# Optimization experiments

Hardware: AMD Instinct MI355X
Metric: run time of the kernel (lower is better)

The kernel has to match this reference:

```python
import jax, jax.numpy as jnp
import numpy as np
import itertools

DIM = 192          # channels
H = W = 64         # input_resolution
WS = 7             # window_size
NH = 6             # num_heads
KD = DIM // NH     # key_dim = 32
D = KD             # attn_ratio=1 -> d = key_dim
DH = D * NH        # 192
B = 16             # batch
HID = int(DIM * 4.0)  # mlp hidden = 768
EPS = 1e-5


def _build_bias_idxs():
    points = list(itertools.product(range(WS), range(WS)))
    offsets, idxs = {}, []
    for p1 in points:
        for p2 in points:
            off = (abs(p1[0] - p2[0]), abs(p1[1] - p2[1]))
            if off not in offsets:
                offsets[off] = len(offsets)
            idxs.append(offsets[off])
    return np.array(idxs, dtype=np.int32).reshape(len(points), len(points)), len(offsets)


def _ln(x, w, b):
    m = x.mean(-1, keepdims=True)
    v = ((x - m) ** 2).mean(-1, keepdims=True)
    return (x - m) * jax.lax.rsqrt(v + EPS) * w + b


def setup_inputs():
    key = jax.random.key(0)
    ks = jax.random.split(key, 20)
    n = lambda k, s, sc=0.02: jax.random.normal(k, s, jnp.float32) * sc
    idxs_np, n_off = _build_bias_idxs()  # [49,49], 49 offsets
    qkv_out = DH + 2 * KD * NH  # 576
    return {
        "x": jax.random.normal(ks[0], (B, H * W, DIM), jnp.float32),
        "ln1_w": jnp.ones((DIM,), jnp.float32),
        "ln1_b": jnp.zeros((DIM,), jnp.float32),
        "qkv_w": n(ks[1], (DIM, qkv_out)),
        "qkv_b": jnp.zeros((qkv_out,), jnp.float32),
        "attn_biases": n(ks[2], (NH, n_off), 0.1),
        "proj_w": n(ks[3], (DH, DIM)),
        "proj_b": jnp.zeros((DIM,), jnp.float32),
        "conv_w": n(ks[4], (DIM, 1, 3, 3), 0.1),  # depthwise OIHW
        "bn_g": jnp.ones((DIM,), jnp.float32),
        "bn_b": jnp.zeros((DIM,), jnp.float32),
        "bn_m": n(ks[5], (DIM,), 0.01),
        "bn_v": jax.random.uniform(ks[6], (DIM,), jnp.float32, 0.5, 1.5),
        "ln2_w": jnp.ones((DIM,), jnp.float32),
        "ln2_b": jnp.zeros((DIM,), jnp.float32),
        "fc1_w": n(ks[7], (DIM, HID)),
        "fc1_b": jnp.zeros((HID,), jnp.float32),
        "fc2_w": n(ks[8], (HID, DIM)),
        "fc2_b": jnp.zeros((DIM,), jnp.float32),
        "bias_idxs": jnp.asarray(idxs_np),
    }


def reference(x, ln1_w, ln1_b, qkv_w, qkv_b, attn_biases, proj_w, proj_b,
              conv_w, bn_g, bn_b, bn_m, bn_v, ln2_w, ln2_b,
              fc1_w, fc1_b, fc2_w, fc2_b, bias_idxs):
    Bn, N, C = x.shape
    shortcut = x

    # ---- window partition (pad 64 -> 70, 10x10 windows of 7x7) ----
    pad = (WS - H % WS) % WS  # 6
    pH = H + pad
    nW = pH // WS  # 10
    xw = x.reshape(Bn, H, W, C)
    xw = jnp.pad(xw, ((0, 0), (0, pad), (0, pad), (0, 0)))
    xw = xw.reshape(Bn, nW, WS, nW, WS, C).transpose(0, 1, 3, 2, 4, 5)
    xw = xw.reshape(Bn * nW * nW, WS * WS, C)  # [1600, 49, C]

    # ---- attention with relative position bias ----
    xn = _ln(xw, ln1_w, ln1_b)
    qkv = xn @ qkv_w + qkv_b                     # [Bw, 49, 576]
    qkv = qkv.reshape(-1, WS * WS, NH, KD + KD + D)
    q, k, v = jnp.split(qkv, [KD, 2 * KD], axis=3)
    q = q.transpose(0, 2, 1, 3)  # [Bw, NH, 49, KD]
    k = k.transpose(0, 2, 1, 3)
    v = v.transpose(0, 2, 1, 3)
    bias = attn_biases[:, bias_idxs]             # [NH, 49, 49]
    attn = jnp.einsum('bhqd,bhkd->bhqk', q, k) * (KD ** -0.5) + bias
    attn = jax.nn.softmax(attn, axis=-1)
    out = jnp.einsum('bhqk,bhkd->bhqd', attn, v)
    out = out.transpose(0, 2, 1, 3).reshape(-1, WS * WS, DH)
    out = out @ proj_w + proj_b                  # [Bw, 49, C]

    # ---- window reverse + unpad ----
    out = out.reshape(Bn, nW, nW, WS, WS, C).transpose(0, 1, 3, 2, 4, 5)
    out = out.reshape(Bn, pH, pH, C)[:, :H, :W].reshape(Bn, N, C)

    x = shortcut + out

    # ---- depthwise local conv + BN (eval) ----
    xc = x.transpose(0, 2, 1).reshape(Bn, C, H, W)
    y = jax.lax.conv_general_dilated(
        xc, conv_w, (1, 1), [(1, 1), (1, 1)],
        dimension_numbers=('NCHW', 'OIHW', 'NCHW'), feature_group_count=C)
    scale = bn_g * jax.lax.rsqrt(bn_v + EPS)
    y = y * scale[None, :, None, None] + (bn_b - bn_m * scale)[None, :, None, None]
    x = y.reshape(Bn, C, N).transpose(0, 2, 1)

    # ---- MLP with pre-LN residual ----
    h = _ln(x, ln2_w, ln2_b)
    h = jax.nn.gelu(h @ fc1_w + fc1_b, approximate=False)
    h = h @ fc2_w + fc2_b
    return x + h
```

## Files before the change

kernel.cpp:

```cpp
#include <hip/hip_runtime.h>
#include <hip/hip_bf16.h>

#define C 192
#define NHh 6
#define NT 49
#define IMG 64
#define WSZ 7

#define XS2 200
#define QKS 392
#define VTS 72
#define PLS 72
#define X3S 200

typedef __attribute__((ext_vector_type(8))) short bf16x8;
typedef __attribute__((ext_vector_type(4))) float f32x4;

__device__ __forceinline__ float bf2f(unsigned short u) {
    union { unsigned int i; float f; } v; v.i = ((unsigned int)u) << 16; return v.f;
}
__device__ __forceinline__ unsigned short f2bf(float f) {
    __hip_bfloat16 h = __float2bfloat16(f);
    return *(unsigned short*)&h;
}
__device__ __forceinline__ float gelu_f(float v) {
    return 0.5f * v * (1.f + erff(v * 0.70710678118654752f));
}

__global__ __launch_bounds__(256) void prep_kernel(
    const float* __restrict__ fc1_w, const float* __restrict__ fc2_w,
    const float* __restrict__ qkv_w, const float* __restrict__ proj_w,
    const float* __restrict__ biases, int noff, const int* __restrict__ bidx,
    const float* __restrict__ bn_g, const float* __restrict__ bn_b,
    const float* __restrict__ bn_m, const float* __restrict__ bn_v,
    unsigned short* __restrict__ wfc1t, unsigned short* __restrict__ wfc2t,
    unsigned short* __restrict__ wqkvt, unsigned short* __restrict__ wprojt,
    float* __restrict__ biasfp, float* __restrict__ bnsc, float* __restrict__ bnsh)
{
    int i = blockIdx.x * 256 + threadIdx.x;
    if (i < 147456) {
        int k = i / 768, n = i - k * 768;
        wfc1t[n * 192 + k] = f2bf(fc1_w[i]);
    } else if (i < 294912) {
        int j = i - 147456;
        int k = j / 192, n = j - k * 192;
        wfc2t[n * 768 + k] = f2bf(fc2_w[j]);
    } else if (i < 405504) {
        int j = i - 294912;
        int k = j / 576, n = j - k * 576;
        wqkvt[n * 192 + k] = f2bf(qkv_w[j]);
    } else if (i < 442368) {
        int j = i - 405504;
        int k = j / 192, n = j - k * 192;
        wprojt[n * 192 + k] = f2bf(proj_w[j]);
    } else if (i < 466944) {
        int j = i - 442368;
        int h = j >> 12, rem = j & 4095;
        int q = rem >> 6, k = rem & 63;
        biasfp[j] = (q < NT && k < NT) ? biases[h * noff + bidx[q * NT + k]] : -1.0e30f;
    } else if (i < 467136) {
        int c = i - 466944;
        float sc = bn_g[c] * rsqrtf(bn_v[c] + 1e-5f);
        bnsc[c] = sc;
        bnsh[c] = bn_b[c] - bn_m[c] * sc;
    }
}

__global__ __launch_bounds__(512) void attn_win_mfma(
    const float* __restrict__ x,
    const float* __restrict__ ln1_w, const float* __restrict__ ln1_b,
    const unsigned short* __restrict__ wqkvt, const float* __restrict__ qkv_b,
    const float* __restrict__ biasfp,
    const unsigned short* __restrict__ wprojt, const float* __restrict__ proj_b,
    unsigned short* __restrict__ x2)
{
    extern __shared__ char smem[];
    unsigned short* xn = (unsigned short*)smem;
    unsigned short* qk = (unsigned short*)(smem + 25600);
    unsigned short* vt = (unsigned short*)(smem + 75776);
    unsigned short* pl = (unsigned short*)(smem + 103424);
    float* stats = (float*)(smem + 121856);

    const int tid = threadIdx.x;
    const int blk = blockIdx.x;
    const int b  = blk / 100;
    const int wi = (blk / 10) % 10;
    const int wj = blk % 10;
    const size_t base = (size_t)b * 4096;
    const int wid = tid >> 6, lane = tid & 63, lr = lane & 15, lg = lane >> 4;

    for (int idx = tid; idx < 64*48; idx += 512) {
        int t = idx / 48, c0 = (idx - t*48) * 4;
        ushort4 sv; sv.x = 0; sv.y = 0; sv.z = 0; sv.w = 0;
        if (t < NT) {
            int gh = wi*WSZ + t/WSZ, gw = wj*WSZ + t%WSZ;
            if (gh < IMG && gw < IMG) {
                float4 v = *(const float4*)(x + (base + (size_t)(gh*IMG + gw))*C + c0);
                sv.x = f2bf(v.x); sv.y = f2bf(v.y); sv.z = f2bf(v.z); sv.w = f2bf(v.w);
            }
        }
        *(ushort4*)&xn[t*XS2 + c0] = sv;
    }
    __syncthreads();

    {
        int lt = tid >> 3, sl = tid & 7;
        float s = 0.f, s2 = 0.f;
        for (int c = sl; c < C; c += 8) {
            float v = bf2f(xn[lt*XS2 + c]);
            s += v; s2 += v*v;
        }
        #pragma unroll
        for (int msk = 1; msk < 8; msk <<= 1) {
            s  += __shfl_xor(s,  msk, 64);
            s2 += __shfl_xor(s2, msk, 64);
        }
        if (sl == 0) {
            float m = s * (1.f/C), var = s2 * (1.f/C) - m*m;
            stats[2*lt]   = m;
            stats[2*lt+1] = rsqrtf(var + 1e-5f);
        }
    }
    __syncthreads();

    for (int idx = tid; idx < 64*48; idx += 512) {
        int t = idx / 48, c0 = (idx - t*48) * 4;
        float mm = stats[2*t], rr = stats[2*t+1];
        ushort4 sv = *(ushort4*)&xn[t*XS2 + c0];
        sv.x = f2bf((bf2f(sv.x) - mm) * rr * ln1_w[c0+0] + ln1_b[c0+0]);
        sv.y = f2bf((bf2f(sv.y) - mm) * rr * ln1_w[c0+1] + ln1_b[c0+1]);
        sv.z = f2bf((bf2f(sv.z) - mm) * rr * ln1_w[c0+2] + ln1_b[c0+2]);
        sv.w = f2bf((bf2f(sv.w) - mm) * rr * ln1_w[c0+3] + ln1_b[c0+3]);
        *(ushort4*)&xn[t*XS2 + c0] = sv;
    }
    __syncthreads();

    for (int nt = wid; nt < 36; nt += 8) {
        const int ncol = nt*16 + lr;
        f32x4 acc0 = {0.f,0.f,0.f,0.f}, acc1 = {0.f,0.f,0.f,0.f};
        f32x4 acc2 = {0.f,0.f,0.f,0.f}, acc3 = {0.f,0.f,0.f,0.f};
        const unsigned short* wp = wqkvt + ncol*192 + lg*8;
        #pragma unroll
        for (int ks = 0; ks < 6; ++ks) {
            bf16x8 bfr = *(const bf16x8*)(wp + ks*32);
            bf16x8 a0 = *(const bf16x8*)(xn + (0*16+lr)*XS2 + ks*32 + lg*8);
            bf16x8 a1 = *(const bf16x8*)(xn + (1*16+lr)*XS2 + ks*32 + lg*8);
            bf16x8 a2 = *(const bf16x8*)(xn + (2*16+lr)*XS2 + ks*32 + lg*8);
            bf16x8 a3 = *(const bf16x8*)(xn + (3*16+lr)*XS2 + ks*32 + lg*8);
            acc0 = __builtin_amdgcn_mfma_f32_16x16x32_bf16(a0, bfr, acc0, 0, 0, 0);
            acc1 = __builtin_amdgcn_mfma_f32_16x16x32_bf16(a1, bfr, acc1, 0, 0, 0);
            acc2 = __builtin_amdgcn_mfma_f32_16x16x32_bf16(a2, bfr, acc2, 0, 0, 0);
            acc3 = __builtin_amdgcn_mfma_f32_16x16x32_bf16(a3, bfr, acc3, 0, 0, 0);
        }
        float bias = qkv_b[ncol];
        const int h = ncol / 96, wo = ncol - h*96;
        #pragma unroll
        for (int mt = 0; mt < 4; ++mt) {
            f32x4 av = (mt==0) ? acc0 : (mt==1) ? acc1 : (mt==2) ? acc2 : acc3;
            #pragma unroll
            for (int r = 0; r < 4; ++r) {
                int tok = mt*16 + lg*4 + r;
                unsigned short v = f2bf(av[r] + bias);
                if (wo < 64) qk[tok*QKS + h*64 + wo] = v;
                else         vt[(h*32 + (wo-64))*VTS + tok] = v;
            }
        }
    }
    __syncthreads();

    unsigned short* ao = xn;
    for (int u = wid; u < 24; u += 8) {
        const int h = u >> 2, nq = u & 3;
        const int qg = nq*16 + lr;
        f32x4 s0 = {0.f,0.f,0.f,0.f}, s1 = {0.f,0.f,0.f,0.f};
        f32x4 s2 = {0.f,0.f,0.f,0.f}, s3 = {0.f,0.f,0.f,0.f};
        bf16x8 qf = *(const bf16x8*)(qk + qg*QKS + h*64 + lg*8);
        bf16x8 k0 = *(const bf16x8*)(qk + (0*16+lr)*QKS + h*64 + 32 + lg*8);
        bf16x8 k1 = *(const bf16x8*)(qk + (1*16+lr)*QKS + h*64 + 32 + lg*8);
        bf16x8 k2 = *(const bf16x8*)(qk + (2*16+lr)*QKS + h*64 + 32 + lg*8);
        bf16x8 k3 = *(const bf16x8*)(qk + (3*16+lr)*QKS + h*64 + 32 + lg*8);
        s0 = __builtin_amdgcn_mfma_f32_16x16x32_bf16(k0, qf, s0, 0, 0, 0);
        s1 = __builtin_amdgcn_mfma_f32_16x16x32_bf16(k1, qf, s1, 0, 0, 0);
        s2 = __builtin_amdgcn_mfma_f32_16x16x32_bf16(k2, qf, s2, 0, 0, 0);
        s3 = __builtin_amdgcn_mfma_f32_16x16x32_bf16(k3, qf, s3, 0, 0, 0);
        const float* bp = biasfp + (size_t)(h*64 + qg)*64 + lg*4;
        float sv[4][4];
        float mx = -3.0e38f;
        #pragma unroll
        for (int mk = 0; mk < 4; ++mk) {
            f32x4 sa = (mk==0) ? s0 : (mk==1) ? s1 : (mk==2) ? s2 : s3;
            float4 b4 = *(const float4*)(bp + mk*16);
            sv[mk][0] = sa[0] * 0.17677669529663687f + b4.x;
            sv[mk][1] = sa[1] * 0.17677669529663687f + b4.y;
            sv[mk][2] = sa[2] * 0.17677669529663687f + b4.z;
            sv[mk][3] = sa[3] * 0.17677669529663687f + b4.w;
            #pragma unroll
            for (int r = 0; r < 4; ++r) mx = fmaxf(mx, sv[mk][r]);
        }
        mx = fmaxf(mx, __shfl_xor(mx, 16, 64));
        mx = fmaxf(mx, __shfl_xor(mx, 32, 64));
        float sum = 0.f;
        #pragma unroll
        for (int mk = 0; mk < 4; ++mk)
            #pragma unroll
            for (int r = 0; r < 4; ++r) { sv[mk][r] = __expf(sv[mk][r] - mx); sum += sv[mk][r]; }
        sum += __shfl_xor(sum, 16, 64);
        sum += __shfl_xor(sum, 32, 64);
        float inv = 1.f / sum;
        unsigned short* pw = pl + (wid*16 + lr)*PLS;
        #pragma unroll
        for (int mk = 0; mk < 4; ++mk)
            #pragma unroll
            for (int r = 0; r < 4; ++r) pw[mk*16 + lg*4 + r] = f2bf(sv[mk][r] * inv);
        #pragma unroll
        for (int dt = 0; dt < 2; ++dt) {
            f32x4 oa = {0.f,0.f,0.f,0.f};
            #pragma unroll
            for (int kk = 0; kk < 2; ++kk) {
                bf16x8 vf = *(const bf16x8*)(vt + (h*32 + dt*16 + lr)*VTS + kk*32 + lg*8);
                bf16x8 pf = *(const bf16x8*)(pl + (wid*16 + lr)*PLS + kk*32 + lg*8);
                oa = __builtin_amdgcn_mfma_f32_16x16x32_bf16(vf, pf, oa, 0, 0, 0);
            }
            #pragma unroll
            for (int r = 0; r < 4; ++r)
                ao[(nq*16 + lr)*XS2 + h*32 + dt*16 + lg*4 + r] = f2bf(oa[r]);
        }
    }
    __syncthreads();

    for (int nt = wid; nt < 12; nt += 8) {
        const int ncol = nt*16 + lr;
        f32x4 acc0 = {0.f,0.f,0.f,0.f}, acc1 = {0.f,0.f,0.f,0.f};
        f32x4 acc2 = {0.f,0.f,0.f,0.f}, acc3 = {0.f,0.f,0.f,0.f};
        const unsigned short* wp = wprojt + ncol*192 + lg*8;
        #pragma unroll
        for (int ks = 0; ks < 6; ++ks) {
            bf16x8 bfr = *(const bf16x8*)(wp + ks*32);
            bf16x8 a0 = *(const bf16x8*)(ao + (0*16+lr)*XS2 + ks*32 + lg*8);
            bf16x8 a1 = *(const bf16x8*)(ao + (1*16+lr)*XS2 + ks*32 + lg*8);
            bf16x8 a2 = *(const bf16x8*)(ao + (2*16+lr)*XS2 + ks*32 + lg*8);
            bf16x8 a3 = *(const bf16x8*)(ao + (3*16+lr)*XS2 + ks*32 + lg*8);
            acc0 = __builtin_amdgcn_mfma_f32_16x16x32_bf16(a0, bfr, acc0, 0, 0, 0);
            acc1 = __builtin_amdgcn_mfma_f32_16x16x32_bf16(a1, bfr, acc1, 0, 0, 0);
            acc2 = __builtin_amdgcn_mfma_f32_16x16x32_bf16(a2, bfr, acc2, 0, 0, 0);
            acc3 = __builtin_amdgcn_mfma_f32_16x16x32_bf16(a3, bfr, acc3, 0, 0, 0);
        }
        float bias = proj_b[ncol];
        #pragma unroll
        for (int mt = 0; mt < 4; ++mt) {
            f32x4 av = (mt==0) ? acc0 : (mt==1) ? acc1 : (mt==2) ? acc2 : acc3;
            #pragma unroll
            for (int r = 0; r < 4; ++r) {
                int tok = mt*16 + lg*4 + r;
                if (tok >= NT) continue;
                int gh = wi*WSZ + tok/WSZ, gw = wj*WSZ + tok%WSZ;
                if (gh >= IMG || gw >= IMG) continue;
                size_t g = (base + (size_t)(gh*IMG + gw))*C + ncol;
                x2[g] = f2bf(av[r] + bias + x[g]);
            }
        }
    }
}

__device__ __forceinline__ f32x4 mfma16(bf16x8 a, bf16x8 b, f32x4 c) {
    return __builtin_amdgcn_mfma_f32_16x16x32_bf16(a, b, c, 0, 0, 0);
}

__device__ __forceinline__ void mlp_produce(
    int ch, unsigned short* buf, const unsigned short* xnl,
    const unsigned short* __restrict__ wfc1t, const float* __restrict__ fc1_b,
    int wid, int lr, int lk)
{
    bf16x8 xa0[6], xa1[6];
    #pragma unroll
    for (int ks = 0; ks < 6; ++ks) {
        xa0[ks] = *(const bf16x8*)(xnl + lr*X3S + ks*32 + lk*8);
        xa1[ks] = *(const bf16x8*)(xnl + (16+lr)*X3S + ks*32 + lk*8);
    }
    #pragma unroll
    for (int t = 0; t < 3; ++t) {
        const int nl = (wid*3 + t)*16 + lr;
        const int ncol = ch*192 + nl;
        f32x4 a0 = {0.f,0.f,0.f,0.f}, a1 = {0.f,0.f,0.f,0.f};
        const unsigned short* wp = wfc1t + (size_t)ncol*192 + lk*8;
        #pragma unroll
        for (int ks = 0; ks < 6; ++ks) {
            bf16x8 bfr = *(const bf16x8*)(wp + ks*32);
            a0 = mfma16(xa0[ks], bfr, a0);
            a1 = mfma16(xa1[ks], bfr, a1);
        }
        float bias = fc1_b[ncol];
        #pragma unroll
        for (int r = 0; r < 4; ++r) {
            int row0 = lk*4 + r;
            buf[row0*X3S + nl]      = f2bf(gelu_f(a0[r] + bias));
            buf[(row0+16)*X3S + nl] = f2bf(gelu_f(a1[r] + bias));
        }
    }
}

__device__ __forceinline__ void mlp_consume(
    int ch, const unsigned short* buf,
    const unsigned short* __restrict__ wfc2t,
    f32x4* acc0, f32x4* acc1, int nb2, int lr, int lk)
{
    #pragma unroll
    for (int ks = 0; ks < 6; ++ks) {
        bf16x8 af0 = *(const bf16x8*)(buf + lr*X3S + ks*32 + lk*8);
        bf16x8 af1 = *(const bf16x8*)(buf + (16+lr)*X3S + ks*32 + lk*8);
        #pragma unroll
        for (int n = 0; n < 3; ++n) {
            bf16x8 b = *(const bf16x8*)(wfc2t + (size_t)(nb2 + n*16 + lr)*768 + ch*192 + ks*32 + lk*8);
            acc0[n] = mfma16(af0, b, acc0[n]);
            acc1[n] = mfma16(af1, b, acc1[n]);
        }
    }
}

__global__ __launch_bounds__(256) void conv_mlp2(
    const unsigned short* __restrict__ x2,
    const float* __restrict__ conv_w,
    const float* __restrict__ bnsc, const float* __restrict__ bnsh,
    const float* __restrict__ ln2_w, const float* __restrict__ ln2_b,
    const unsigned short* __restrict__ wfc1t, const float* __restrict__ fc1_b,
    const unsigned short* __restrict__ wfc2t, const float* __restrict__ fc2_b,
    float* __restrict__ out)
{
    extern __shared__ char smem[];
    unsigned short* x3  = (unsigned short*)smem;
    unsigned short* xnl = (unsigned short*)(smem + 12800);
    unsigned short* h1a = (unsigned short*)(smem + 25600);
    unsigned short* h1b = (unsigned short*)(smem + 38400);
    float* stats = (float*)(smem + 51200);

    const int tid  = threadIdx.x;
    const int base = blockIdx.x * 32;
    const int b    = base >> 12;
    const int n0   = base & 4095;
    const int hh   = n0 >> 6;
    const int w0v  = n0 & 63;
    const size_t ibase = (size_t)b * 4096;

    for (int idx = tid; idx < 32*48; idx += 256) {
        int lt = idx / 48, c0 = (idx - lt*48) * 4;
        int ww = w0v + lt;
        float a0 = 0.f, a1 = 0.f, a2 = 0.f, a3 = 0.f;
        #pragma unroll
        for (int kh = -1; kh <= 1; ++kh) {
            int h2 = hh + kh;
            if (h2 < 0 || h2 >= IMG) continue;
            #pragma unroll
            for (int kw = -1; kw <= 1; ++kw) {
                int w2 = ww + kw;
                if (w2 < 0 || w2 >= IMG) continue;
                ushort4 v = *(const ushort4*)(x2 + (ibase + (size_t)(h2*IMG + w2))*C + c0);
                int tap = (kh+1)*3 + (kw+1);
                a0 += bf2f(v.x) * conv_w[(c0+0)*9 + tap];
                a1 += bf2f(v.y) * conv_w[(c0+1)*9 + tap];
                a2 += bf2f(v.z) * conv_w[(c0+2)*9 + tap];
                a3 += bf2f(v.w) * conv_w[(c0+3)*9 + tap];
            }
        }
        ushort4 o;
        o.x = f2bf(a0 * bnsc[c0+0] + bnsh[c0+0]);
        o.y = f2bf(a1 * bnsc[c0+1] + bnsh[c0+1]);
        o.z = f2bf(a2 * bnsc[c0+2] + bnsh[c0+2]);
        o.w = f2bf(a3 * bnsc[c0+3] + bnsh[c0+3]);
        *(ushort4*)&x3[lt*X3S + c0] = o;
    }
    __syncthreads();

    {
        int lt = tid >> 3, sl = tid & 7;
        float s = 0.f, s2 = 0.f;
        for (int c = sl; c < C; c += 8) {
            float v = bf2f(x3[lt*X3S + c]);
            s += v; s2 += v*v;
        }
        #pragma unroll
        for (int msk = 1; msk < 8; msk <<= 1) {
            s  += __shfl_xor(s,  msk, 64);
            s2 += __shfl_xor(s2, msk, 64);
        }
        if (sl == 0) {
            float m = s * (1.f/C), var = s2 * (1.f/C) - m*m;
            stats[2*lt]   = m;
            stats[2*lt+1] = rsqrtf(var + 1e-5f);
        }
    }
    __syncthreads();

    for (int idx = tid; idx < 32*48; idx += 256) {
        int lt = idx / 48, c0 = (idx - lt*48) * 4;
        float mm = stats[2*lt], rr = stats[2*lt+1];
        ushort4 v = *(ushort4*)&x3[lt*X3S + c0];
        ushort4 sv;
        sv.x = f2bf((bf2f(v.x) - mm) * rr * ln2_w[c0+0] + ln2_b[c0+0]);
        sv.y = f2bf((bf2f(v.y) - mm) * rr * ln2_w[c0+1] + ln2_b[c0+1]);
        sv.z = f2bf((bf2f(v.z) - mm) * rr * ln2_w[c0+2] + ln2_b[c0+2]);
        sv.w = f2bf((bf2f(v.w) - mm) * rr * ln2_w[c0+3] + ln2_b[c0+3]);
        *(ushort4*)&xnl[lt*XS2 + c0] = sv;
    }
    __syncthreads();

    const int wid = tid >> 6, l = tid & 63, lr = l & 15, lk = l >> 4;
    const int nb2 = wid * 48;

    f32x4 acc0[3] = {{0.f,0.f,0.f,0.f},{0.f,0.f,0.f,0.f},{0.f,0.f,0.f,0.f}};
    f32x4 acc1[3] = {{0.f,0.f,0.f,0.f},{0.f,0.f,0.f,0.f},{0.f,0.f,0.f,0.f}};

    mlp_produce(0, h1a, xnl, wfc1t, fc1_b, wid, lr, lk);
    __syncthreads();

    mlp_produce(1, h1b, xnl, wfc1t, fc1_b, wid, lr, lk);
    mlp_consume(0, h1a, wfc2t, acc0, acc1, nb2, lr, lk);
    __syncthreads();

    mlp_produce(2, h1a, xnl, wfc1t, fc1_b, wid, lr, lk);
    mlp_consume(1, h1b, wfc2t, acc0, acc1, nb2, lr, lk);
    __syncthreads();

    mlp_produce(3, h1b, xnl, wfc1t, fc1_b, wid, lr, lk);
    mlp_consume(2, h1a, wfc2t, acc0, acc1, nb2, lr, lk);
    __syncthreads();

    mlp_consume(3, h1b, wfc2t, acc0, acc1, nb2, lr, lk);

    #pragma unroll
    for (int n = 0; n < 3; ++n) {
        int col = nb2 + n*16 + lr;
        float bias = fc2_b[col];
        #pragma unroll
        for (int r = 0; r < 4; ++r) {
            int row0 = lk*4 + r;
            float v0 = acc0[n][r] + bias + bf2f(x3[row0*X3S + col]);
            float v1 = acc1[n][r] + bias + bf2f(x3[(row0+16)*X3S + col]);
            out[(size_t)(base + row0) * C + col]      = v0;
            out[(size_t)(base + row0 + 16) * C + col] = v1;
        }
    }
}

extern "C" void kernel_launch(void* const* d_in, const int* in_sizes, int n_in,
                              void* d_out, int out_size, void* d_ws, size_t ws_size,
                              hipStream_t stream)
{
    const float* x      = (const float*)d_in[0];
    const float* ln1_w  = (const float*)d_in[1];
    const float* ln1_b  = (const float*)d_in[2];
    const float* qkv_w  = (const float*)d_in[3];
    const float* qkv_b  = (const float*)d_in[4];
    const float* biases = (const float*)d_in[5];
    const float* proj_w = (const float*)d_in[6];
    const float* proj_b = (const float*)d_in[7];
    const float* conv_w = (const float*)d_in[8];
    const float* bn_g   = (const float*)d_in[9];
    const float* bn_b   = (const float*)d_in[10];
    const float* bn_m   = (const float*)d_in[11];
    const float* bn_v   = (const float*)d_in[12];
    const float* ln2_w  = (const float*)d_in[13];
    const float* ln2_b  = (const float*)d_in[14];
    const float* fc1_w  = (const float*)d_in[15];
    const float* fc1_b  = (const float*)d_in[16];
    const float* fc2_w  = (const float*)d_in[17];
    const float* fc2_b  = (const float*)d_in[18];
    const int* bidx     = (const int*)d_in[19];

    char* ws = (char*)d_ws;
    unsigned short* x2    = (unsigned short*)ws;
    unsigned short* wfc1t = (unsigned short*)(ws + 25165824);
    unsigned short* wfc2t = (unsigned short*)(ws + 25460736);
    unsigned short* wqkvt = (unsigned short*)(ws + 25755648);
    unsigned short* wprojt= (unsigned short*)(ws + 25976832);
    float*          biasfp= (float*)(ws + 26050560);
    float*          bnsc  = (float*)(ws + 26148864);
    float*          bnsh  = (float*)(ws + 26149632);
    float* out = (float*)d_out;
    int noff = in_sizes[5] / NHh;

    prep_kernel<<<(467136 + 255)/256, 256, 0, stream>>>(
        fc1_w, fc2_w, qkv_w, proj_w, biases, noff, bidx,
        bn_g, bn_b, bn_m, bn_v,
        wfc1t, wfc2t, wqkvt, wprojt, biasfp, bnsc, bnsh);

    size_t smem1 = 122368;
    hipFuncSetAttribute((const void*)attn_win_mfma,
                        hipFuncAttributeMaxDynamicSharedMemorySize, (int)smem1);
    attn_win_mfma<<<16*100, 512, smem1, stream>>>(
        x, ln1_w, ln1_b, wqkvt, qkv_b, biasfp, wprojt, proj_b, x2);

    size_t smem2 = 51456;
    hipFuncSetAttribute((const void*)conv_mlp2,
                        hipFuncAttributeMaxDynamicSharedMemorySize, (int)smem2);
    conv_mlp2<<<65536/32, 256, smem2, stream>>>(
        x2, conv_w, bnsc, bnsh, ln2_w, ln2_b,
        wfc1t, fc1_b, wfc2t, fc2_b, out);
}
```

Measured before the change: 552.2 us.

## Tile-transpose weight prep, keep conv output in registers, stash residual in output

```diff
diff --git a/kernel.cpp b/kernel.cpp
--- a/kernel.cpp
+++ b/kernel.cpp
@@ -33,36 +33,56 @@
     const float* __restrict__ biases, int noff, const int* __restrict__ bidx,
     const float* __restrict__ bn_g, const float* __restrict__ bn_b,
     const float* __restrict__ bn_m, const float* __restrict__ bn_v,
+    const float* __restrict__ conv_w,
     unsigned short* __restrict__ wfc1t, unsigned short* __restrict__ wfc2t,
     unsigned short* __restrict__ wqkvt, unsigned short* __restrict__ wprojt,
-    float* __restrict__ biasfp, float* __restrict__ bnsc, float* __restrict__ bnsh)
+    float* __restrict__ biasfp, float* __restrict__ bnsc, float* __restrict__ bnsh,
+    float* __restrict__ convwt)
 {
-    int i = blockIdx.x * 256 + threadIdx.x;
-    if (i < 147456) {
-        int k = i / 768, n = i - k * 768;
-        wfc1t[n * 192 + k] = f2bf(fc1_w[i]);
-    } else if (i < 294912) {
-        int j = i - 147456;
-        int k = j / 192, n = j - k * 192;
-        wfc2t[n * 768 + k] = f2bf(fc2_w[j]);
-    } else if (i < 405504) {
-        int j = i - 294912;
-        int k = j / 576, n = j - k * 576;
-        wqkvt[n * 192 + k] = f2bf(qkv_w[j]);
-    } else if (i < 442368) {
-        int j = i - 405504;
-        int k = j / 192, n = j - k * 192;
-        wprojt[n * 192 + k] = f2bf(proj_w[j]);
-    } else if (i < 466944) {
-        int j = i - 442368;
-        int h = j >> 12, rem = j & 4095;
-        int q = rem >> 6, k = rem & 63;
-        biasfp[j] = (q < NT && k < NT) ? biases[h * noff + bidx[q * NT + k]] : -1.0e30f;
-    } else if (i < 467136) {
-        int c = i - 466944;
-        float sc = bn_g[c] * rsqrtf(bn_v[c] + 1e-5f);
-        bnsc[c] = sc;
-        bnsh[c] = bn_b[c] - bn_m[c] * sc;
+    __shared__ unsigned short tbuf[64 * 68];
+    const int bid = blockIdx.x, tid = threadIdx.x;
+
+    if (bid < 108) {
+        const float* src; unsigned short* dst; int K, N, tk, tn;
+        if (bid < 36)      { src = fc1_w;  dst = wfc1t;  K = 192; N = 768; tk = bid/12;      tn = bid%12; }
+        else if (bid < 72) { src = fc2_w;  dst = wfc2t;  K = 768; N = 192; tk = (bid-36)/3;  tn = (bid-36)%3; }
+        else if (bid < 99) { src = qkv_w;  dst = wqkvt;  K = 192; N = 576; tk = (bid-72)/9;  tn = (bid-72)%9; }
+        else               { src = proj_w; dst = wprojt; K = 192; N = 192; tk = (bid-99)/3;  tn = (bid-99)%3; }
+        for (int i = tid; i < 1024; i += 256) {
+            int r = i >> 4, c = (i & 15) * 4;
+            float4 v = *(const float4*)(src + (size_t)(tk*64 + r) * N + tn*64 + c);
+            ushort4 s; s.x = f2bf(v.x); s.y = f2bf(v.y); s.z = f2bf(v.z); s.w = f2bf(v.w);
+            *(ushort4*)&tbuf[r*68 + c] = s;
+        }
+        __syncthreads();
+        for (int i = tid; i < 1024; i += 256) {
+            int n = i >> 4, k = (i & 15) * 4;
+            ushort4 o;
+            o.x = tbuf[(k+0)*68 + n];
+            o.y = tbuf[(k+1)*68 + n];
+            o.z = tbuf[(k+2)*68 + n];
+            o.w = tbuf[(k+3)*68 + n];
+            *(ushort4*)(dst + (size_t)(tn*64 + n) * K + tk*64 + k) = o;
+        }
+    } else if (bid < 204) {
+        int j = (bid - 108) * 256 + tid;
+        if (j < 24576) {
+            int h = j >> 12, rem = j & 4095;
+            int q = rem >> 6, k = rem & 63;
+            biasfp[j] = (q < NT && k < NT) ? biases[h * noff + bidx[q * NT + k]] : -1.0e30f;
+        }
+    } else {
+        for (int it = tid; it < 1920; it += 256) {
+            if (it < 192) {
+                float sc = bn_g[it] * rsqrtf(bn_v[it] + 1e-5f);
+                bnsc[it] = sc;
+                bnsh[it] = bn_b[it] - bn_m[it] * sc;
+            } else {
+                int idx = it - 192;
+                int tap = idx / 192, c = idx - tap * 192;
+                convwt[tap * 192 + c] = conv_w[c * 9 + tap];
+            }
+        }
     }
 }
 
@@ -317,21 +337,19 @@
     }
 }
 
-__global__ __launch_bounds__(256) void conv_mlp2(
+__global__ __launch_bounds__(256, 4) void conv_mlp3(
     const unsigned short* __restrict__ x2,
-    const float* __restrict__ conv_w,
+    const float* __restrict__ convwt,
     const float* __restrict__ bnsc, const float* __restrict__ bnsh,
     const float* __restrict__ ln2_w, const float* __restrict__ ln2_b,
     const unsigned short* __restrict__ wfc1t, const float* __restrict__ fc1_b,
     const unsigned short* __restrict__ wfc2t, const float* __restrict__ fc2_b,
-    float* __restrict__ out)
+    float* out)
 {
     extern __shared__ char smem[];
-    unsigned short* x3  = (unsigned short*)smem;
-    unsigned short* xnl = (unsigned short*)(smem + 12800);
-    unsigned short* h1a = (unsigned short*)(smem + 25600);
-    unsigned short* h1b = (unsigned short*)(smem + 38400);
-    float* stats = (float*)(smem + 51200);
+    unsigned short* xnl = (unsigned short*)smem;
+    unsigned short* h1a = (unsigned short*)(smem + 12800);
+    unsigned short* h1b = (unsigned short*)(smem + 25600);
 
     const int tid  = threadIdx.x;
     const int base = blockIdx.x * 32;
@@ -341,10 +359,12 @@
     const int w0v  = n0 & 63;
     const size_t ibase = (size_t)b * 4096;
 
-    for (int idx = tid; idx < 32*48; idx += 256) {
-        int lt = idx / 48, c0 = (idx - lt*48) * 4;
-        int ww = w0v + lt;
-        float a0 = 0.f, a1 = 0.f, a2 = 0.f, a3 = 0.f;
+    {
+        const int lt = tid >> 3, sl = tid & 7;
+        const int ww = w0v + lt;
+        float4 xv[6];
+        #pragma unroll
+        for (int j = 0; j < 6; ++j) { xv[j].x = 0.f; xv[j].y = 0.f; xv[j].z = 0.f; xv[j].w = 0.f; }
         #pragma unroll
         for (int kh = -1; kh <= 1; ++kh) {
             int h2 = hh + kh;
@@ -353,53 +373,53 @@
             for (int kw = -1; kw <= 1; ++kw) {
                 int w2 = ww + kw;
                 if (w2 < 0 || w2 >= IMG) continue;
-                ushort4 v = *(const ushort4*)(x2 + (ibase + (size_t)(h2*IMG + w2))*C + c0);
-                int tap = (kh+1)*3 + (kw+1);
-                a0 += bf2f(v.x) * conv_w[(c0+0)*9 + tap];
-                a1 += bf2f(v.y) * conv_w[(c0+1)*9 + tap];
-                a2 += bf2f(v.z) * conv_w[(c0+2)*9 + tap];
-                a3 += bf2f(v.w) * conv_w[(c0+3)*9 + tap];
+                const unsigned short* src = x2 + (ibase + (size_t)(h2*IMG + w2))*C;
+                const float* wt = convwt + ((kh+1)*3 + (kw+1)) * 192;
+                #pragma unroll
+                for (int j = 0; j < 6; ++j) {
+                    int c0 = (sl + 8*j) * 4;
+                    ushort4 v = *(const ushort4*)(src + c0);
+                    float4 w = *(const float4*)(wt + c0);
+                    xv[j].x += bf2f(v.x) * w.x;
+                    xv[j].y += bf2f(v.y) * w.y;
+                    xv[j].z += bf2f(v.z) * w.z;
+                    xv[j].w += bf2f(v.w) * w.w;
+                }
             }
         }
-        ushort4 o;
-        o.x = f2bf(a0 * bnsc[c0+0] + bnsh[c0+0]);
-        o.y = f2bf(a1 * bnsc[c0+1] + bnsh[c0+1]);
-        o.z = f2bf(a2 * bnsc[c0+2] + bnsh[c0+2]);
-        o.w = f2bf(a3 * bnsc[c0+3] + bnsh[c0+3]);
-        *(ushort4*)&x3[lt*X3S + c0] = o;
-    }
-    __syncthreads();
-
-    {
-        int lt = tid >> 3, sl = tid & 7;
         float s = 0.f, s2 = 0.f;
-        for (int c = sl; c < C; c += 8) {
-            float v = bf2f(x3[lt*X3S + c]);
-            s += v; s2 += v*v;
+        #pragma unroll
+        for (int j = 0; j < 6; ++j) {
+            int c0 = (sl + 8*j) * 4;
+            float4 sc = *(const float4*)(bnsc + c0);
+            float4 sh = *(const float4*)(bnsh + c0);
+            xv[j].x = xv[j].x * sc.x + sh.x;
+            xv[j].y = xv[j].y * sc.y + sh.y;
+            xv[j].z = xv[j].z * sc.z + sh.z;
+            xv[j].w = xv[j].w * sc.w + sh.w;
+            *(float4*)(out + ((size_t)base + lt)*C + c0) = xv[j];
+            s  += xv[j].x + xv[j].y + xv[j].z + xv[j].w;
+            s2 += xv[j].x*xv[j].x + xv[j].y*xv[j].y + xv[j].z*xv[j].z + xv[j].w*xv[j].w;
         }
         #pragma unroll
         for (int msk = 1; msk < 8; msk <<= 1) {
             s  += __shfl_xor(s,  msk, 64);
             s2 += __shfl_xor(s2, msk, 64);
         }
-        if (sl == 0) {
-            float m = s * (1.f/C), var = s2 * (1.f/C) - m*m;
-            stats[2*lt]   = m;
-            stats[2*lt+1] = rsqrtf(var + 1e-5f);
-        }
-    }
-    __syncthreads();
-
-    for (int idx = tid; idx < 32*48; idx += 256) {
-        int lt = idx / 48, c0 = (idx - lt*48) * 4;
-        float mm = stats[2*lt], rr = stats[2*lt+1];
-        ushort4 v = *(ushort4*)&x3[lt*X3S + c0];
-        ushort4 sv;
-        sv.x = f2bf((bf2f(v.x) - mm) * rr * ln2_w[c0+0] + ln2_b[c0+0]);
-        sv.y = f2bf((bf2f(v.y) - mm) * rr * ln2_w[c0+1] + ln2_b[c0+1]);
-        sv.z = f2bf((bf2f(v.z) - mm) * rr * ln2_w[c0+2] + ln2_b[c0+2]);
-        sv.w = f2bf((bf2f(v.w) - mm) * rr * ln2_w[c0+3] + ln2_b[c0+3]);
-        *(ushort4*)&xnl[lt*XS2 + c0] = sv;
+        float m = s * (1.f/C), var = s2 * (1.f/C) - m*m;
+        float rs = rsqrtf(var + 1e-5f);
+        #pragma unroll
+        for (int j = 0; j < 6; ++j) {
+            int c0 = (sl + 8*j) * 4;
+            float4 lw = *(const float4*)(ln2_w + c0);
+            float4 lb = *(const float4*)(ln2_b + c0);
+            ushort4 sv;
+            sv.x = f2bf((xv[j].x - m) * rs * lw.x + lb.x);
+            sv.y = f2bf((xv[j].y - m) * rs * lw.y + lb.y);
+            sv.z = f2bf((xv[j].z - m) * rs * lw.z + lb.z);
+            sv.w = f2bf((xv[j].w - m) * rs * lw.w + lb.w);
+            *(ushort4*)&xnl[lt*X3S + c0] = sv;
+        }
     }
     __syncthreads();
 
@@ -411,19 +431,15 @@
 
     mlp_produce(0, h1a, xnl, wfc1t, fc1_b, wid, lr, lk);
     __syncthreads();
-
     mlp_produce(1, h1b, xnl, wfc1t, fc1_b, wid, lr, lk);
     mlp_consume(0, h1a, wfc2t, acc0, acc1, nb2, lr, lk);
     __syncthreads();
-
     mlp_produce(2, h1a, xnl, wfc1t, fc1_b, wid, lr, lk);
     mlp_consume(1, h1b, wfc2t, acc0, acc1, nb2, lr, lk);
     __syncthreads();
-
     mlp_produce(3, h1b, xnl, wfc1t, fc1_b, wid, lr, lk);
     mlp_consume(2, h1a, wfc2t, acc0, acc1, nb2, lr, lk);
     __syncthreads();
-
     mlp_consume(3, h1b, wfc2t, acc0, acc1, nb2, lr, lk);
 
     #pragma unroll
@@ -433,10 +449,12 @@
         #pragma unroll
         for (int r = 0; r < 4; ++r) {
             int row0 = lk*4 + r;
-            float v0 = acc0[n][r] + bias + bf2f(x3[row0*X3S + col]);
-            float v1 = acc1[n][r] + bias + bf2f(x3[(row0+16)*X3S + col]);
-            out[(size_t)(base + row0) * C + col]      = v0;
-            out[(size_t)(base + row0 + 16) * C + col] = v1;
+            size_t g0 = (size_t)(base + row0) * C + col;
+            size_t g1 = (size_t)(base + row0 + 16) * C + col;
+            float v0 = acc0[n][r] + bias + out[g0];
+            float v1 = acc1[n][r] + bias + out[g1];
+            out[g0] = v0;
+            out[g1] = v1;
         }
     }
 }
@@ -475,13 +493,14 @@
     float*          biasfp= (float*)(ws + 26050560);
     float*          bnsc  = (float*)(ws + 26148864);
     float*          bnsh  = (float*)(ws + 26149632);
+    float*          convwt= (float*)(ws + 26150400);
     float* out = (float*)d_out;
     int noff = in_sizes[5] / NHh;
 
-    prep_kernel<<<(467136 + 255)/256, 256, 0, stream>>>(
+    prep_kernel<<<205, 256, 0, stream>>>(
         fc1_w, fc2_w, qkv_w, proj_w, biases, noff, bidx,
-        bn_g, bn_b, bn_m, bn_v,
-        wfc1t, wfc2t, wqkvt, wprojt, biasfp, bnsc, bnsh);
+        bn_g, bn_b, bn_m, bn_v, conv_w,
+        wfc1t, wfc2t, wqkvt, wprojt, biasfp, bnsc, bnsh, convwt);
 
     size_t smem1 = 122368;
     hipFuncSetAttribute((const void*)attn_win_mfma,
@@ -489,10 +508,10 @@
     attn_win_mfma<<<16*100, 512, smem1, stream>>>(
         x, ln1_w, ln1_b, wqkvt, qkv_b, biasfp, wprojt, proj_b, x2);
 
-    size_t smem2 = 51456;
-    hipFuncSetAttribute((const void*)conv_mlp2,
+    size_t smem2 = 38400;
+    hipFuncSetAttribute((const void*)conv_mlp3,
                         hipFuncAttributeMaxDynamicSharedMemorySize, (int)smem2);
-    conv_mlp2<<<65536/32, 256, smem2, stream>>>(
-        x2, conv_w, bnsc, bnsh, ln2_w, ln2_b,
+    conv_mlp3<<<65536/32, 256, smem2, stream>>>(
+        x2, convwt, bnsc, bnsh, ln2_w, ln2_b,
         wfc1t, fc1_b, wfc2t, fc2_b, out);
 }
```

Result: faster. 453.5 us (-17.9%).
